# Kernel optimization log

Hardware: AMD Instinct MI355X
Metric: run time of the kernel (lower is better)

## Reference

```python
import jax, jax.numpy as jnp
import numpy as np

S = 14
STEP = 1.0 / S
LAMBDA_COORD = 7.0
LAMBDA_NOOBJ = 0.2
LAMBDA_CLS = 1.5
EPS = 1e-06


def _xywh_to_xyxy(box):
    # box: [N, S, S, 2, 4]; grid offset i = column (axis 2), j = row (axis 1)
    gx = jnp.arange(S, dtype=box.dtype)[None, None, :, None]
    gy = jnp.arange(S, dtype=box.dtype)[None, :, None, None]
    x = (box[..., 0] + gx) * STEP
    y = (box[..., 1] + gy) * STEP
    w = box[..., 2]
    h = box[..., 3]
    return jnp.stack([x - w / 2, y - h / 2, x + w / 2, y + h / 2], axis=-1)


def _iou(b1, b2):
    # b1, b2: [..., 4] xyxy, elementwise IoU
    x1 = jnp.maximum(b1[..., 0], b2[..., 0])
    y1 = jnp.maximum(b1[..., 1], b2[..., 1])
    x2 = jnp.minimum(b1[..., 2], b2[..., 2])
    y2 = jnp.minimum(b1[..., 3], b2[..., 3])
    inter = jnp.maximum(x2 - x1, 0.0) * jnp.maximum(y2 - y1, 0.0)
    area1 = (b1[..., 2] - b1[..., 0]) * (b1[..., 3] - b1[..., 1])
    area2 = (b2[..., 2] - b2[..., 0]) * (b2[..., 3] - b2[..., 1])
    union = area1 + area2 - inter + EPS
    return inter / union


def _ciou_loss(b1, b2):
    # b1 = pred xyxy, b2 = target xyxy (both already include grid offsets)
    iou = _iou(b1, b2)
    cx1 = (b1[..., 0] + b1[..., 2]) / 2
    cy1 = (b1[..., 1] + b1[..., 3]) / 2
    cx2 = (b2[..., 0] + b2[..., 2]) / 2
    cy2 = (b2[..., 1] + b2[..., 3]) / 2
    center_dist = (cx1 - cx2) ** 2 + (cy1 - cy2) ** 2
    x_c1 = jnp.minimum(b1[..., 0], b2[..., 0])
    y_c1 = jnp.minimum(b1[..., 1], b2[..., 1])
    x_c2 = jnp.maximum(b1[..., 2], b2[..., 2])
    y_c2 = jnp.maximum(b1[..., 3], b2[..., 3])
    outer_diag = (x_c2 - x_c1) ** 2 + (y_c2 - y_c1) ** 2 + EPS
    w1 = jnp.maximum(b1[..., 2] - b1[..., 0], EPS)
    h1 = jnp.maximum(b1[..., 3] - b1[..., 1], EPS)
    w2 = jnp.maximum(b2[..., 2] - b2[..., 0], EPS)
    h2 = jnp.maximum(b2[..., 3] - b2[..., 1], EPS)
    v = 4.0 / (jnp.pi ** 2) * (jnp.arctan(w2 / h2) - jnp.arctan(w1 / h1)) ** 2
    alpha = v / (1.0 - iou + v + EPS)
    ciou = iou - center_dist / outer_diag - alpha * v
    scale = jnp.maximum(2.0 - w2 * h2, 1.0)
    return (1.0 - ciou) * scale


def setup_inputs() -> dict:
    key = jax.random.key(0)
    k1, k2, k3 = jax.random.split(key, 3)
    N = 4096
    pred = jax.random.uniform(k1, (N, S, S, 30), dtype=jnp.float32)
    target = jax.random.uniform(k2, (N, S, S, 30), dtype=jnp.float32)
    # both anchor boxes of a cell share the same objectness, as in YOLOv1 encoding.
    obj_cell = jax.random.uniform(k3, (N, S, S)) < 0.1
    conf0 = jnp.where(obj_cell, jnp.maximum(target[..., 4], 0.5), 0.0)
    conf1 = jnp.where(obj_cell, jnp.maximum(target[..., 9], 0.5), 0.0)
    target = target.at[..., 4].set(conf0).at[..., 9].set(conf1)
    return {"pred": pred, "target": target}


def reference(pred, target):
    N = pred.shape[0]
    tb = target[..., :10].reshape(N, S, S, 2, 5)
    pb = pred[..., :10].reshape(N, S, S, 2, 5)
    tcls = target[..., 10:]
    pcls = pred[..., 10:]

    obj = tb[..., 4] > 0            # [N,S,S,2]
    sig = obj[..., 1]               # [N,S,S]

    b1 = _xywh_to_xyxy(pb[..., :4])  # pred
    b2 = _xywh_to_xyxy(tb[..., :4])  # target

    # responsible box per object cell: argmax IoU over the 2 predictors
    iou = _iou(b1, b2)               # [N,S,S,2]
    resp = jnp.argmax(iou, axis=-1)  # [N,S,S]
    suppress = sig[..., None] & (jnp.arange(2) == (1 - resp)[..., None])
    obj_m = obj & ~suppress
    noobj_m = ~obj_m

    dconf = (pb[..., 4] - tb[..., 4]) ** 2
    obj_loss = jnp.sum(jnp.where(obj_m, dconf, 0.0))
    noobj_loss = jnp.sum(jnp.where(noobj_m, dconf, 0.0))

    ciou = _ciou_loss(b1, b2)        # [N,S,S,2]
    bbox_loss = jnp.sum(jnp.where(sig[..., None] & obj_m, ciou, 0.0))

    p = jnp.clip(pcls, 1e-07, 1.0 - 1e-07)
    bce = -(tcls * jnp.log(p) + (1.0 - tcls) * jnp.log1p(-p))
    class_loss = jnp.sum(jnp.where(sig[..., None], bce, 0.0)) * LAMBDA_CLS

    loss = obj_loss + LAMBDA_NOOBJ * noobj_loss + LAMBDA_COORD * bbox_loss + class_loss
    return loss / N
```

## Files before the change

kernel.cpp:

```cpp
#include <hip/hip_runtime.h>
#include <stdint.h>

#define S 14
#define NBATCH 4096
#define TOTAL (NBATCH * S * S)
#define CPB   128
#define TPB   256
#define GRID  (TOTAL / CPB)
#define TILE_BYTES_TENSOR (CPB * 30 * 4)
#define CHUNKS_PER_TENSOR (TILE_BYTES_TENSOR / 1024)
#define CHUNKS_TOTAL (CHUNKS_PER_TENSOR * 2)

constexpr float STEP_C       = 1.0f / 14.0f;
constexpr float EPS_C        = 1e-6f;
constexpr float LAMBDA_NOOBJ = 0.2f;
constexpr float LAMBDA_COORD = 7.0f;
constexpr float LAMBDA_CLS   = 1.5f;
constexpr float INV_N        = 1.0f / (float)NBATCH;
constexpr float C_V          = 0.40528473456935109f;

__device__ __forceinline__ void gload_lds16(const void* gsrc, void* lds_dst) {
    __builtin_amdgcn_global_load_lds(
        (const __attribute__((address_space(1))) void*)gsrc,
        (__attribute__((address_space(3))) void*)lds_dst,
        16, 0, 0);
}

__global__ __launch_bounds__(TPB) void yolo_loss_kernel(
    const float* __restrict__ pred, const float* __restrict__ target,
    float* __restrict__ partial) {
    __shared__ char sbuf[2 * TILE_BYTES_TENSOR];
    __shared__ float ws[4];

    const int tid  = threadIdx.x;
    const int lane = tid & 63;
    const int wid  = tid >> 6;

    const size_t blockByte = (size_t)blockIdx.x * TILE_BYTES_TENSOR;
    const char* gpred = reinterpret_cast<const char*>(pred)   + blockByte;
    const char* gtarg = reinterpret_cast<const char*>(target) + blockByte;

    #pragma unroll
    for (int i = 0; i < 8; ++i) {
        int c = wid * 8 + i;
        if (c < CHUNKS_TOTAL) {
            const char* gsrc = (c < CHUNKS_PER_TENSOR)
                ? gpred + (size_t)c * 1024
                : gtarg + (size_t)(c - CHUNKS_PER_TENSOR) * 1024;
            gload_lds16(gsrc + lane * 16, sbuf + c * 1024);
        }
    }
    __syncthreads();

    const float* sp = reinterpret_cast<const float*>(sbuf);
    const float* st = reinterpret_cast<const float*>(sbuf + TILE_BYTES_TENSOR);

    float contrib = 0.0f;
    float d0 = 0.0f, d1 = 0.0f;
    bool  sig = false;
    const int rbase = tid * 30;

    if (tid < CPB) {
        float t4 = st[rbase + 4], t9 = st[rbase + 9];
        float p4 = sp[rbase + 4], p9 = sp[rbase + 9];
        d0 = p4 - t4;
        d1 = p9 - t9;
        sig = t4 > 0.0f;
        contrib = LAMBDA_NOOBJ * (d0 * d0 + d1 * d1);
    }

    unsigned long long mask = __ballot(sig);
    int nsig = __popcll(mask);

    __shared__ int slist[4][64];
    if (sig) {
        int rank = __popcll(mask & ((1ull << lane) - 1ull));
        slist[wid][rank] = tid;

        int cell = blockIdx.x * CPB + tid;
        int j = cell % S;
        int i = (cell / S) % S;
        float gx = (float)j, gy = (float)i;

        float p0 = sp[rbase + 0], p1 = sp[rbase + 1], p2 = sp[rbase + 2], p3 = sp[rbase + 3];
        float p5 = sp[rbase + 5], p6 = sp[rbase + 6], p7 = sp[rbase + 7], p8 = sp[rbase + 8];
        float t0 = st[rbase + 0], t1 = st[rbase + 1], t2 = st[rbase + 2], t3 = st[rbase + 3];
        float t5 = st[rbase + 5], t6 = st[rbase + 6], t7 = st[rbase + 7], t8 = st[rbase + 8];

        float P0x = (p0 + gx) * STEP_C, P0y = (p1 + gy) * STEP_C;
        float P1x = (p5 + gx) * STEP_C, P1y = (p6 + gy) * STEP_C;
        float T0x = (t0 + gx) * STEP_C, T0y = (t1 + gy) * STEP_C;
        float T1x = (t5 + gx) * STEP_C, T1y = (t6 + gy) * STEP_C;

        float a0x0 = P0x - p2 * 0.5f, a0y0 = P0y - p3 * 0.5f;
        float a0x1 = P0x + p2 * 0.5f, a0y1 = P0y + p3 * 0.5f;
        float a1x0 = P1x - p7 * 0.5f, a1y0 = P1y - p8 * 0.5f;
        float a1x1 = P1x + p7 * 0.5f, a1y1 = P1y + p8 * 0.5f;
        float b0x0 = T0x - t2 * 0.5f, b0y0 = T0y - t3 * 0.5f;
        float b0x1 = T0x + t2 * 0.5f, b0y1 = T0y + t3 * 0.5f;
        float b1x0 = T1x - t7 * 0.5f, b1y0 = T1y - t8 * 0.5f;
        float b1x1 = T1x + t7 * 0.5f, b1y1 = T1y + t8 * 0.5f;

        float i0x1 = fmaxf(a0x0, b0x0), i0y1 = fmaxf(a0y0, b0y0);
        float i0x2 = fminf(a0x1, b0x1), i0y2 = fminf(a0y1, b0y1);
        float inter0 = fmaxf(i0x2 - i0x1, 0.0f) * fmaxf(i0y2 - i0y1, 0.0f);
        float ar0a = (a0x1 - a0x0) * (a0y1 - a0y0);
        float ar0b = (b0x1 - b0x0) * (b0y1 - b0y0);
        float iou0 = inter0 / (ar0a + ar0b - inter0 + EPS_C);

        float i1x1 = fmaxf(a1x0, b1x0), i1y1 = fmaxf(a1y0, b1y0);
        float i1x2 = fminf(a1x1, b1x1), i1y2 = fminf(a1y1, b1y1);
        float inter1 = fmaxf(i1x2 - i1x1, 0.0f) * fmaxf(i1y2 - i1y1, 0.0f);
        float ar1a = (a1x1 - a1x0) * (a1y1 - a1y0);
        float ar1b = (b1x1 - b1x0) * (b1y1 - b1y0);
        float iou1 = inter1 / (ar1a + ar1b - inter1 + EPS_C);

        bool r1 = iou1 > iou0;

        float dr = r1 ? d1 : d0;
        contrib += (1.0f - LAMBDA_NOOBJ) * dr * dr;

        float ax0 = r1 ? a1x0 : a0x0, ay0 = r1 ? a1y0 : a0y0;
        float ax1 = r1 ? a1x1 : a0x1, ay1 = r1 ? a1y1 : a0y1;
        float bx0 = r1 ? b1x0 : b0x0, by0 = r1 ? b1y0 : b0y0;
        float bx1 = r1 ? b1x1 : b0x1, by1 = r1 ? b1y1 : b0y1;
        float iou = r1 ? iou1 : iou0;

        float cx1 = (ax0 + ax1) * 0.5f, cy1 = (ay0 + ay1) * 0.5f;
        float cx2 = (bx0 + bx1) * 0.5f, cy2 = (by0 + by1) * 0.5f;
        float cd = (cx1 - cx2) * (cx1 - cx2) + (cy1 - cy2) * (cy1 - cy2);
        float xc1 = fminf(ax0, bx0), yc1 = fminf(ay0, by0);
        float xc2 = fmaxf(ax1, bx1), yc2 = fmaxf(ay1, by1);
        float od = (xc2 - xc1) * (xc2 - xc1) + (yc2 - yc1) * (yc2 - yc1) + EPS_C;
        float w1 = fmaxf(ax1 - ax0, EPS_C), h1 = fmaxf(ay1 - ay0, EPS_C);
        float w2 = fmaxf(bx1 - bx0, EPS_C), h2 = fmaxf(by1 - by0, EPS_C);
        float dd = atanf(w2 / h2) - atanf(w1 / h1);
        float vv = C_V * dd * dd;
        float alpha = vv / (1.0f - iou + vv + EPS_C);
        float ciou = iou - cd / od - alpha * vv;
        float scale = fmaxf(2.0f - w2 * h2, 1.0f);
        contrib += LAMBDA_COORD * (1.0f - ciou) * scale;
    }

    __syncthreads();

    {
        float s = 0.0f;
        int nitems = nsig * 20;
        for (int q = lane; q < nitems; q += 64) {
            int ciq = q / 20;
            int cls = q - ciq * 20;
            int r2  = slist[wid][ciq];
            float pc = sp[r2 * 30 + 10 + cls];
            float tc = st[r2 * 30 + 10 + cls];
            pc = fminf(fmaxf(pc, 1e-7f), 1.0f - 1e-7f);
            s += tc * logf(pc) + (1.0f - tc) * log1pf(-pc);
        }
        contrib -= LAMBDA_CLS * s;
    }

    float r = contrib;
    #pragma unroll
    for (int off = 32; off > 0; off >>= 1) r += __shfl_down(r, off);

    if (lane == 0) ws[wid] = r;
    __syncthreads();
    if (tid == 0)
        partial[blockIdx.x] = ws[0] + ws[1] + ws[2] + ws[3];
}

__global__ __launch_bounds__(256) void yolo_reduce_kernel(
    const float* __restrict__ partial, float* __restrict__ out) {
    const int tid  = threadIdx.x;
    const int lane = tid & 63;
    const int wid  = tid >> 6;

    float s = 0.0f;
    for (int i = tid; i < GRID; i += 256) s += partial[i];

    #pragma unroll
    for (int off = 32; off > 0; off >>= 1) s += __shfl_down(s, off);

    __shared__ float ws[4];
    if (lane == 0) ws[wid] = s;
    __syncthreads();
    if (tid == 0)
        out[0] = (ws[0] + ws[1] + ws[2] + ws[3]) * INV_N;
}

extern "C" void kernel_launch(void* const* d_in, const int* in_sizes, int n_in,
                              void* d_out, int out_size, void* d_ws, size_t ws_size,
                              hipStream_t stream) {
    const float* pred   = (const float*)d_in[0];
    const float* target = (const float*)d_in[1];
    float* out     = (float*)d_out;
    float* partial = (float*)d_ws;

    hipLaunchKernelGGL(yolo_loss_kernel, dim3(GRID), dim3(TPB), 0, stream,
                       pred, target, partial);
    hipLaunchKernelGGL(yolo_reduce_kernel, dim3(1), dim3(256), 0, stream,
                       partial, out);
}
```

Measured before the change: 42.93 us.

## Switch to single-wave blocks with double-buffered multi-tile LDS staging

Measured after the change: 67.86 us. 58.1% more time.

```diff
diff --git a/kernel.cpp b/kernel.cpp
--- a/kernel.cpp
+++ b/kernel.cpp
@@ -4,12 +4,13 @@
 #define S 14
 #define NBATCH 4096
 #define TOTAL (NBATCH * S * S)
-#define CPB   128
-#define TPB   256
+#define TPB   64
+#define TILE_CELLS 128
+#define NT    4
+#define CPB   (TILE_CELLS * NT)
 #define GRID  (TOTAL / CPB)
-#define TILE_BYTES_TENSOR (CPB * 30 * 4)
-#define CHUNKS_PER_TENSOR (TILE_BYTES_TENSOR / 1024)
-#define CHUNKS_TOTAL (CHUNKS_PER_TENSOR * 2)
+#define TILE_TB (TILE_CELLS * 120)
+#define NCHUNK  (TILE_TB / 1024)
 
 constexpr float STEP_C       = 1.0f / 14.0f;
 constexpr float EPS_C        = 1e-6f;
@@ -19,154 +20,158 @@
 constexpr float INV_N        = 1.0f / (float)NBATCH;
 constexpr float C_V          = 0.40528473456935109f;
 
-__device__ __forceinline__ void gload_lds16(const void* gsrc, void* lds_dst) {
+__device__ __forceinline__ void gload16(const char* gsrc, char* lds_dst) {
     __builtin_amdgcn_global_load_lds(
         (const __attribute__((address_space(1))) void*)gsrc,
         (__attribute__((address_space(3))) void*)lds_dst,
         16, 0, 0);
 }
 
+__device__ __forceinline__ void stage_tile(const char* gp, const char* gt,
+                                           int t, char* buf, int lane) {
+    const char* ps = gp + (size_t)t * TILE_TB + lane * 16;
+    const char* ts = gt + (size_t)t * TILE_TB + lane * 16;
+    #pragma unroll
+    for (int c = 0; c < NCHUNK; ++c) gload16(ps + c * 1024, buf + c * 1024);
+    #pragma unroll
+    for (int c = 0; c < NCHUNK; ++c) gload16(ts + c * 1024, buf + TILE_TB + c * 1024);
+}
+
 __global__ __launch_bounds__(TPB) void yolo_loss_kernel(
     const float* __restrict__ pred, const float* __restrict__ target,
     float* __restrict__ partial) {
-    __shared__ char sbuf[2 * TILE_BYTES_TENSOR];
-    __shared__ float ws[4];
-
-    const int tid  = threadIdx.x;
-    const int lane = tid & 63;
-    const int wid  = tid >> 6;
-
-    const size_t blockByte = (size_t)blockIdx.x * TILE_BYTES_TENSOR;
-    const char* gpred = reinterpret_cast<const char*>(pred)   + blockByte;
-    const char* gtarg = reinterpret_cast<const char*>(target) + blockByte;
-
-    #pragma unroll
-    for (int i = 0; i < 8; ++i) {
-        int c = wid * 8 + i;
-        if (c < CHUNKS_TOTAL) {
-            const char* gsrc = (c < CHUNKS_PER_TENSOR)
-                ? gpred + (size_t)c * 1024
-                : gtarg + (size_t)(c - CHUNKS_PER_TENSOR) * 1024;
-            gload_lds16(gsrc + lane * 16, sbuf + c * 1024);
+    __shared__ __align__(16) char sbuf[2][2 * TILE_TB];
+    __shared__ int slist[2][64];
+
+    const int lane = threadIdx.x;
+    const char* gp = reinterpret_cast<const char*>(pred)   + (size_t)blockIdx.x * NT * TILE_TB;
+    const char* gt = reinterpret_cast<const char*>(target) + (size_t)blockIdx.x * NT * TILE_TB;
+
+    float contrib = 0.0f;
+
+    stage_tile(gp, gt, 0, sbuf[0], lane);
+
+    for (int t = 0; t < NT; ++t) {
+        if (t + 1 < NT) stage_tile(gp, gt, t + 1, sbuf[(t + 1) & 1], lane);
+
+        if (t + 1 < NT) asm volatile("s_waitcnt vmcnt(30)" ::: "memory");
+        else            asm volatile("s_waitcnt vmcnt(0)"  ::: "memory");
+        __builtin_amdgcn_sched_barrier(0);
+
+        const float* sp = reinterpret_cast<const float*>(sbuf[t & 1]);
+        const float* st = reinterpret_cast<const float*>(sbuf[t & 1] + TILE_TB);
+
+        #pragma unroll
+        for (int sub = 0; sub < 2; ++sub) {
+            const int rbase = (sub * 64 + lane) * 30;
+
+            float t4 = st[rbase + 4], t9 = st[rbase + 9];
+            float p4 = sp[rbase + 4], p9 = sp[rbase + 9];
+            float d0 = p4 - t4;
+            float d1 = p9 - t9;
+            bool  sig = t4 > 0.0f;
+            contrib += LAMBDA_NOOBJ * (d0 * d0 + d1 * d1);
+
+            unsigned long long mask = __ballot(sig);
+            int nsig = __popcll(mask);
+
+            if (sig) {
+                int rank = __popcll(mask & ((1ull << lane) - 1ull));
+                slist[sub][rank] = sub * 64 + lane;
+
+                int cell = (blockIdx.x * NT + t) * TILE_CELLS + sub * 64 + lane;
+                int j = cell % S;
+                int i = (cell / S) % S;
+                float gx = (float)j, gy = (float)i;
+
+                float p0 = sp[rbase + 0], p1 = sp[rbase + 1], p2 = sp[rbase + 2], p3 = sp[rbase + 3];
+                float p5 = sp[rbase + 5], p6 = sp[rbase + 6], p7 = sp[rbase + 7], p8 = sp[rbase + 8];
+                float t0 = st[rbase + 0], t1 = st[rbase + 1], t2 = st[rbase + 2], t3 = st[rbase + 3];
+                float t5 = st[rbase + 5], t6 = st[rbase + 6], t7 = st[rbase + 7], t8 = st[rbase + 8];
+
+                float P0x = (p0 + gx) * STEP_C, P0y = (p1 + gy) * STEP_C;
+                float P1x = (p5 + gx) * STEP_C, P1y = (p6 + gy) * STEP_C;
+                float T0x = (t0 + gx) * STEP_C, T0y = (t1 + gy) * STEP_C;
+                float T1x = (t5 + gx) * STEP_C, T1y = (t6 + gy) * STEP_C;
+
+                float a0x0 = P0x - p2 * 0.5f, a0y0 = P0y - p3 * 0.5f;
+                float a0x1 = P0x + p2 * 0.5f, a0y1 = P0y + p3 * 0.5f;
+                float a1x0 = P1x - p7 * 0.5f, a1y0 = P1y - p8 * 0.5f;
+                float a1x1 = P1x + p7 * 0.5f, a1y1 = P1y + p8 * 0.5f;
+                float b0x0 = T0x - t2 * 0.5f, b0y0 = T0y - t3 * 0.5f;
+                float b0x1 = T0x + t2 * 0.5f, b0y1 = T0y + t3 * 0.5f;
+                float b1x0 = T1x - t7 * 0.5f, b1y0 = T1y - t8 * 0.5f;
+                float b1x1 = T1x + t7 * 0.5f, b1y1 = T1y + t8 * 0.5f;
+
+                float i0x1 = fmaxf(a0x0, b0x0), i0y1 = fmaxf(a0y0, b0y0);
+                float i0x2 = fminf(a0x1, b0x1), i0y2 = fminf(a0y1, b0y1);
+                float inter0 = fmaxf(i0x2 - i0x1, 0.0f) * fmaxf(i0y2 - i0y1, 0.0f);
+                float ar0a = (a0x1 - a0x0) * (a0y1 - a0y0);
+                float ar0b = (b0x1 - b0x0) * (b0y1 - b0y0);
+                float iou0 = inter0 / (ar0a + ar0b - inter0 + EPS_C);
+
+                float i1x1 = fmaxf(a1x0, b1x0), i1y1 = fmaxf(a1y0, b1y0);
+                float i1x2 = fminf(a1x1, b1x1), i1y2 = fminf(a1y1, b1y1);
+                float inter1 = fmaxf(i1x2 - i1x1, 0.0f) * fmaxf(i1y2 - i1y1, 0.0f);
+                float ar1a = (a1x1 - a1x0) * (a1y1 - a1y0);
+                float ar1b = (b1x1 - b1x0) * (b1y1 - b1y0);
+                float iou1 = inter1 / (ar1a + ar1b - inter1 + EPS_C);
+
+                bool r1 = iou1 > iou0;
+
+                float dr = r1 ? d1 : d0;
+                contrib += (1.0f - LAMBDA_NOOBJ) * dr * dr;
+
+                float ax0 = r1 ? a1x0 : a0x0, ay0 = r1 ? a1y0 : a0y0;
+                float ax1 = r1 ? a1x1 : a0x1, ay1 = r1 ? a1y1 : a0y1;
+                float bx0 = r1 ? b1x0 : b0x0, by0 = r1 ? b1y0 : b0y0;
+                float bx1 = r1 ? b1x1 : b0x1, by1 = r1 ? b1y1 : b0y1;
+                float iou = r1 ? iou1 : iou0;
+
+                float cx1 = (ax0 + ax1) * 0.5f, cy1 = (ay0 + ay1) * 0.5f;
+                float cx2 = (bx0 + bx1) * 0.5f, cy2 = (by0 + by1) * 0.5f;
+                float cd = (cx1 - cx2) * (cx1 - cx2) + (cy1 - cy2) * (cy1 - cy2);
+                float xc1 = fminf(ax0, bx0), yc1 = fminf(ay0, by0);
+                float xc2 = fmaxf(ax1, bx1), yc2 = fmaxf(ay1, by1);
+                float od = (xc2 - xc1) * (xc2 - xc1) + (yc2 - yc1) * (yc2 - yc1) + EPS_C;
+                float w1 = fmaxf(ax1 - ax0, EPS_C), h1 = fmaxf(ay1 - ay0, EPS_C);
+                float w2 = fmaxf(bx1 - bx0, EPS_C), h2 = fmaxf(by1 - by0, EPS_C);
+                float dd = atanf(w2 / h2) - atanf(w1 / h1);
+                float vv = C_V * dd * dd;
+                float alpha = vv / (1.0f - iou + vv + EPS_C);
+                float ciou = iou - cd / od - alpha * vv;
+                float scale = fmaxf(2.0f - w2 * h2, 1.0f);
+                contrib += LAMBDA_COORD * (1.0f - ciou) * scale;
+            }
+
+            asm volatile("s_waitcnt lgkmcnt(0)" ::: "memory");
+            __builtin_amdgcn_sched_barrier(0);
+
+            {
+                float s = 0.0f;
+                int nitems = nsig * 20;
+                for (int q = lane; q < nitems; q += 64) {
+                    int ciq = q / 20;
+                    int cls = q - ciq * 20;
+                    int r2  = slist[sub][ciq] * 30 + 10 + cls;
+                    float pc = sp[r2];
+                    float tc = st[r2];
+                    pc = fminf(fmaxf(pc, 1e-7f), 1.0f - 1e-7f);
+                    s += tc * logf(pc) + (1.0f - tc) * log1pf(-pc);
+                }
+                contrib -= LAMBDA_CLS * s;
+            }
         }
+
+        asm volatile("s_waitcnt lgkmcnt(0)" ::: "memory");
+        __builtin_amdgcn_sched_barrier(0);
     }
-    __syncthreads();
-
-    const float* sp = reinterpret_cast<const float*>(sbuf);
-    const float* st = reinterpret_cast<const float*>(sbuf + TILE_BYTES_TENSOR);
-
-    float contrib = 0.0f;
-    float d0 = 0.0f, d1 = 0.0f;
-    bool  sig = false;
-    const int rbase = tid * 30;
-
-    if (tid < CPB) {
-        float t4 = st[rbase + 4], t9 = st[rbase + 9];
-        float p4 = sp[rbase + 4], p9 = sp[rbase + 9];
-        d0 = p4 - t4;
-        d1 = p9 - t9;
-        sig = t4 > 0.0f;
-        contrib = LAMBDA_NOOBJ * (d0 * d0 + d1 * d1);
-    }
-
-    unsigned long long mask = __ballot(sig);
-    int nsig = __popcll(mask);
-
-    __shared__ int slist[4][64];
-    if (sig) {
-        int rank = __popcll(mask & ((1ull << lane) - 1ull));
-        slist[wid][rank] = tid;
-
-        int cell = blockIdx.x * CPB + tid;
-        int j = cell % S;
-        int i = (cell / S) % S;
-        float gx = (float)j, gy = (float)i;
-
-        float p0 = sp[rbase + 0], p1 = sp[rbase + 1], p2 = sp[rbase + 2], p3 = sp[rbase + 3];
-        float p5 = sp[rbase + 5], p6 = sp[rbase + 6], p7 = sp[rbase + 7], p8 = sp[rbase + 8];
-        float t0 = st[rbase + 0], t1 = st[rbase + 1], t2 = st[rbase + 2], t3 = st[rbase + 3];
-        float t5 = st[rbase + 5], t6 = st[rbase + 6], t7 = st[rbase + 7], t8 = st[rbase + 8];
-
-        float P0x = (p0 + gx) * STEP_C, P0y = (p1 + gy) * STEP_C;
-        float P1x = (p5 + gx) * STEP_C, P1y = (p6 + gy) * STEP_C;
-        float T0x = (t0 + gx) * STEP_C, T0y = (t1 + gy) * STEP_C;
-        float T1x = (t5 + gx) * STEP_C, T1y = (t6 + gy) * STEP_C;
-
-        float a0x0 = P0x - p2 * 0.5f, a0y0 = P0y - p3 * 0.5f;
-        float a0x1 = P0x + p2 * 0.5f, a0y1 = P0y + p3 * 0.5f;
-        float a1x0 = P1x - p7 * 0.5f, a1y0 = P1y - p8 * 0.5f;
-        float a1x1 = P1x + p7 * 0.5f, a1y1 = P1y + p8 * 0.5f;
-        float b0x0 = T0x - t2 * 0.5f, b0y0 = T0y - t3 * 0.5f;
-        float b0x1 = T0x + t2 * 0.5f, b0y1 = T0y + t3 * 0.5f;
-        float b1x0 = T1x - t7 * 0.5f, b1y0 = T1y - t8 * 0.5f;
-        float b1x1 = T1x + t7 * 0.5f, b1y1 = T1y + t8 * 0.5f;
-
-        float i0x1 = fmaxf(a0x0, b0x0), i0y1 = fmaxf(a0y0, b0y0);
-        float i0x2 = fminf(a0x1, b0x1), i0y2 = fminf(a0y1, b0y1);
-        float inter0 = fmaxf(i0x2 - i0x1, 0.0f) * fmaxf(i0y2 - i0y1, 0.0f);
-        float ar0a = (a0x1 - a0x0) * (a0y1 - a0y0);
-        float ar0b = (b0x1 - b0x0) * (b0y1 - b0y0);
-        float iou0 = inter0 / (ar0a + ar0b - inter0 + EPS_C);
-
-        float i1x1 = fmaxf(a1x0, b1x0), i1y1 = fmaxf(a1y0, b1y0);
-        float i1x2 = fminf(a1x1, b1x1), i1y2 = fminf(a1y1, b1y1);
-        float inter1 = fmaxf(i1x2 - i1x1, 0.0f) * fmaxf(i1y2 - i1y1, 0.0f);
-        float ar1a = (a1x1 - a1x0) * (a1y1 - a1y0);
-        float ar1b = (b1x1 - b1x0) * (b1y1 - b1y0);
-        float iou1 = inter1 / (ar1a + ar1b - inter1 + EPS_C);
-
-        bool r1 = iou1 > iou0;
-
-        float dr = r1 ? d1 : d0;
-        contrib += (1.0f - LAMBDA_NOOBJ) * dr * dr;
-
-        float ax0 = r1 ? a1x0 : a0x0, ay0 = r1 ? a1y0 : a0y0;
-        float ax1 = r1 ? a1x1 : a0x1, ay1 = r1 ? a1y1 : a0y1;
-        float bx0 = r1 ? b1x0 : b0x0, by0 = r1 ? b1y0 : b0y0;
-        float bx1 = r1 ? b1x1 : b0x1, by1 = r1 ? b1y1 : b0y1;
-        float iou = r1 ? iou1 : iou0;
-
-        float cx1 = (ax0 + ax1) * 0.5f, cy1 = (ay0 + ay1) * 0.5f;
-        float cx2 = (bx0 + bx1) * 0.5f, cy2 = (by0 + by1) * 0.5f;
-        float cd = (cx1 - cx2) * (cx1 - cx2) + (cy1 - cy2) * (cy1 - cy2);
-        float xc1 = fminf(ax0, bx0), yc1 = fminf(ay0, by0);
-        float xc2 = fmaxf(ax1, bx1), yc2 = fmaxf(ay1, by1);
-        float od = (xc2 - xc1) * (xc2 - xc1) + (yc2 - yc1) * (yc2 - yc1) + EPS_C;
-        float w1 = fmaxf(ax1 - ax0, EPS_C), h1 = fmaxf(ay1 - ay0, EPS_C);
-        float w2 = fmaxf(bx1 - bx0, EPS_C), h2 = fmaxf(by1 - by0, EPS_C);
-        float dd = atanf(w2 / h2) - atanf(w1 / h1);
-        float vv = C_V * dd * dd;
-        float alpha = vv / (1.0f - iou + vv + EPS_C);
-        float ciou = iou - cd / od - alpha * vv;
-        float scale = fmaxf(2.0f - w2 * h2, 1.0f);
-        contrib += LAMBDA_COORD * (1.0f - ciou) * scale;
-    }
-
-    __syncthreads();
-
-    {
-        float s = 0.0f;
-        int nitems = nsig * 20;
-        for (int q = lane; q < nitems; q += 64) {
-            int ciq = q / 20;
-            int cls = q - ciq * 20;
-            int r2  = slist[wid][ciq];
-            float pc = sp[r2 * 30 + 10 + cls];
-            float tc = st[r2 * 30 + 10 + cls];
-            pc = fminf(fmaxf(pc, 1e-7f), 1.0f - 1e-7f);
-            s += tc * logf(pc) + (1.0f - tc) * log1pf(-pc);
-        }
-        contrib -= LAMBDA_CLS * s;
-    }
 
     float r = contrib;
     #pragma unroll
     for (int off = 32; off > 0; off >>= 1) r += __shfl_down(r, off);
-
-    if (lane == 0) ws[wid] = r;
-    __syncthreads();
-    if (tid == 0)
-        partial[blockIdx.x] = ws[0] + ws[1] + ws[2] + ws[3];
+    if (lane == 0)
+        partial[blockIdx.x] = r;
 }
 
 __global__ __launch_bounds__(256) void yolo_reduce_kernel(
```
